# Performance work log

Hardware: AMD Instinct MI355X
Metric: run time of the kernel (lower is better)

## Reference

```python
import jax, jax.numpy as jnp
import numpy as np

IH, IW = 14, 14
NUM_HEADS = 16
HEAD_DIMS = 32
INP_DIMS = 512
B = 128


def make_relative_position_index(ih, iw):
    coords = np.stack(np.meshgrid(np.arange(ih), np.arange(iw), indexing='ij'))  # [2, ih, iw]
    cf = coords.reshape(2, -1)  # [2, n]
    rel = cf[:, :, None] - cf[:, None, :]  # [2, n, n]
    rel = rel.transpose(1, 2, 0)  # [n, n, 2]
    rel[:, :, 0] += ih - 1
    rel[:, :, 1] += iw - 1
    rel[:, :, 0] *= 2 * iw - 1
    return rel.sum(-1).astype(np.int64)  # [n, n]


def setup_inputs() -> dict:
    key = jax.random.key(0)
    k1, k2, k3, k4, k5 = jax.random.split(key, 5)
    n = IH * IW
    inner = NUM_HEADS * HEAD_DIMS
    x = jax.random.normal(k1, (B, n, INP_DIMS), dtype=jnp.float32)
    qkv_w = jax.random.normal(k2, (INP_DIMS, 3 * inner), dtype=jnp.float32) * 0.02
    rel_bias_table = jax.random.normal(k3, ((2 * IH - 1) * (2 * IW - 1), NUM_HEADS), dtype=jnp.float32) * 0.02
    proj_w = jax.random.normal(k4, (inner, INP_DIMS), dtype=jnp.float32) * 0.02
    proj_b = jax.random.normal(k5, (INP_DIMS,), dtype=jnp.float32) * 0.02
    rel_pos_index = jnp.asarray(make_relative_position_index(IH, IW))
    return {"x": x, "qkv_w": qkv_w, "rel_bias_table": rel_bias_table,
            "proj_w": proj_w, "proj_b": proj_b, "rel_pos_index": rel_pos_index}


def reference(x, qkv_w, rel_bias_table, proj_w, proj_b, rel_pos_index):
    b, n, c = x.shape
    h, hd = NUM_HEADS, HEAD_DIMS
    scale = (INP_DIMS // NUM_HEADS) ** (-0.5)
    qkv = x @ qkv_w  # [b, n, 3*h*hd]
    qkv = qkv.reshape(b, n, 3, h, hd).transpose(2, 0, 3, 1, 4)  # [3, b, h, n, hd]
    q, k, v = qkv[0] * scale, qkv[1], qkv[2]
    attn = jnp.einsum('bhqd,bhkd->bhqk', q, k)  # [b, h, n, n]
    # gather relative position bias: [n*n, h] -> [h, n, n]
    bias = rel_bias_table[rel_pos_index.reshape(-1)].reshape(n, n, h).transpose(2, 0, 1)
    attn = jax.nn.softmax(attn + bias[None], axis=-1)
    out = jnp.einsum('bhqk,bhkd->bhqd', attn, v)  # [b, h, n, hd]
    out = out.transpose(0, 2, 1, 3).reshape(b, n, h * hd)
    return out @ proj_w + proj_b
```

## Files before the change

### kernel.cpp

```cpp
#include <hip/hip_runtime.h>

#define NTOK 196
#define QPAD 208
#define KP 208
#define PSTR 232

typedef __attribute__((ext_vector_type(8))) short short8;
typedef __attribute__((ext_vector_type(4))) float float4_t;

__device__ __forceinline__ short f2bf(float f) {
  unsigned u = __float_as_uint(f);
  u = (u + 0x7fffu + ((u >> 16) & 1u)) >> 16;
  return (short)u;
}

__global__ __launch_bounds__(256) void fill_kernel(float* __restrict__ out,
                                                   int n) {
  int i = blockIdx.x * 256 + threadIdx.x;
  if (i < n) out[i] = 1000.0f;
}

__global__ __launch_bounds__(256) void cvt_kernel(const float* __restrict__ in,
                                                  short* __restrict__ out) {
  int i = (blockIdx.x * 256 + threadIdx.x) * 8;
  float4_t a = *(const float4_t*)&in[i];
  float4_t b = *(const float4_t*)&in[i + 4];
  short8 v;
  v[0] = f2bf(a[0]); v[1] = f2bf(a[1]); v[2] = f2bf(a[2]); v[3] = f2bf(a[3]);
  v[4] = f2bf(b[0]); v[5] = f2bf(b[1]); v[6] = f2bf(b[2]); v[7] = f2bf(b[3]);
  *(short8*)&out[i] = v;
}

__global__ __launch_bounds__(256) void transpose_kernel(
    const float* __restrict__ in, short* __restrict__ out, int R, int C) {
  __shared__ float tile[64][65];
  int c0 = blockIdx.x * 64, r0 = blockIdx.y * 64;
  int tc = threadIdx.x & 63, tr = threadIdx.x >> 6;
#pragma unroll
  for (int s = 0; s < 16; s++) {
    int r = s * 4 + tr;
    tile[r][tc] = in[(r0 + r) * C + c0 + tc];
  }
  __syncthreads();
#pragma unroll
  for (int s = 0; s < 16; s++) {
    int i = s * 4 + tr;
    out[(c0 + i) * R + r0 + tc] = f2bf(tile[tc][i]);
  }
}

__global__ __launch_bounds__(256) void bias_kernel(
    const float* __restrict__ table, const int* __restrict__ rpi,
    float* __restrict__ bias) {
  int idx = blockIdx.x * 256 + threadIdx.x;
  if (idx >= 16 * QPAD * KP) return;
  int h = idx / (QPAD * KP);
  int rem = idx % (QPAD * KP);
  int q = rem / KP, k = rem % KP;
  float v = 0.f;
  if (q < NTOK && k < NTOK) v = table[rpi[q * NTOK + k] * 16 + h];
  bias[idx] = v;
}

__global__ __launch_bounds__(256, 2) void fused_attn(
    const short* __restrict__ xb, const short* __restrict__ wt1,
    const float* __restrict__ bias, short* __restrict__ aout) {
  __shared__ __align__(16) short R1[64 * PSTR];
  __shared__ __align__(16) short R2[32 * PSTR];
  __shared__ __align__(16) short Qs[224][40];
  __shared__ __align__(16) short Ks[224][40];
  short(*As)[40] = (short(*)[40])R1;
  short(*P)[PSTR] = (short(*)[PSTR])R1;
  short(*Bs)[40] = (short(*)[40])R2;
  short(*vTs)[PSTR] = (short(*)[PSTR])R2;

  int bh = blockIdx.x, b = bh >> 4, h = bh & 15;
  int tid = threadIdx.x, wave = tid >> 6, lane = tid & 63;
  int quad = lane >> 4, l16 = lane & 15;
  int base_row = b * NTOK;

  float4_t z4 = {0.f, 0.f, 0.f, 0.f};
  float4_t acc[4][6];
#pragma unroll
  for (int i = 0; i < 4; i++)
#pragma unroll
    for (int n = 0; n < 6; n++) acc[i][n] = z4;

  int srow = tid >> 2, scol = (tid & 3) * 8;
  for (int k0 = 0; k0 < 512; k0 += 32) {
#pragma unroll
    for (int i = 0; i < 4; i++) {
      int r = srow + i * 64;
      if (r < 224) {
        int gr = base_row + r;
        if (gr > 25087) gr = 25087;
        *(short8*)&As[r][scol] = *(const short8*)&xb[gr * 512 + k0 + scol];
      }
    }
#pragma unroll
    for (int i = 0; i < 2; i++) {
      int r = srow + i * 64;
      if (r < 96) {
        int sec = r >> 5, r32 = r & 31;
        *(short8*)&Bs[r][scol] =
            *(const short8*)&wt1[(sec * 512 + h * 32 + r32) * 512 + k0 + scol];
      }
    }
    __syncthreads();
    short8 af[4], bfv[6];
#pragma unroll
    for (int i = 0; i < 4; i++) {
      int mt = (i < 3) ? (wave + 4 * i) : (12 + (wave & 1));
      af[i] = *(short8*)&As[mt * 16 + l16][quad * 8];
    }
#pragma unroll
    for (int n = 0; n < 6; n++) bfv[n] = *(short8*)&Bs[n * 16 + l16][quad * 8];
#pragma unroll
    for (int i = 0; i < 4; i++)
#pragma unroll
      for (int n = 0; n < 6; n++)
        acc[i][n] = __builtin_amdgcn_mfma_f32_16x16x32_bf16(af[i], bfv[n],
                                                            acc[i][n], 0, 0, 0);
    __syncthreads();
  }
  const float qscale = 0.17677669529663687f;
#pragma unroll
  for (int i = 0; i < 4; i++) {
    if (i == 3 && wave >= 2) break;
    int mt = (i < 3) ? (wave + 4 * i) : (12 + wave);
    int row0 = mt * 16 + quad * 4;
#pragma unroll
    for (int n = 0; n < 6; n++) {
      int c = n * 16 + l16;
#pragma unroll
      for (int r = 0; r < 4; r++) {
        int row = row0 + r;
        float v = acc[i][n][r];
        if (c < 32)
          Qs[row][c] = f2bf(v * qscale);
        else if (c < 64)
          Ks[row][c - 32] = f2bf(v);
        else
          vTs[c - 64][row] = f2bf(v);
      }
    }
  }
  __syncthreads();
  for (int i2 = 0; i2 < 4; i2++) {
    bool active = (i2 < 3) || (wave == 0);
    int qt = (i2 < 3) ? (wave + 4 * i2) : 12;
    int qr0 = qt * 16;
    if (active) {
      short8 qf = *(short8*)&Qs[qr0 + l16][quad * 8];
      float4_t s[13];
#pragma unroll
      for (int kt = 0; kt < 13; kt++) {
        short8 kf = *(short8*)&Ks[kt * 16 + l16][quad * 8];
        s[kt] = __builtin_amdgcn_mfma_f32_16x16x32_bf16(qf, kf, z4, 0, 0, 0);
      }
      const float* brow = bias + (h * QPAD + qr0 + quad * 4) * KP;
#pragma unroll
      for (int kt = 0; kt < 13; kt++) {
        int col = kt * 16 + l16;
#pragma unroll
        for (int r = 0; r < 4; r++) s[kt][r] += brow[r * KP + col];
      }
      if (l16 >= 4) {
#pragma unroll
        for (int r = 0; r < 4; r++) s[12][r] = -1e30f;
      }
      int prow_base = wave * 16 + quad * 4;
#pragma unroll
      for (int r = 0; r < 4; r++) {
        float m = s[0][r];
#pragma unroll
        for (int kt = 1; kt < 13; kt++) m = fmaxf(m, s[kt][r]);
        m = fmaxf(m, __shfl_xor(m, 8, 16));
        m = fmaxf(m, __shfl_xor(m, 4, 16));
        m = fmaxf(m, __shfl_xor(m, 2, 16));
        m = fmaxf(m, __shfl_xor(m, 1, 16));
        float sum = 0.f;
#pragma unroll
        for (int kt = 0; kt < 13; kt++) {
          float p = __expf(s[kt][r] - m);
          s[kt][r] = p;
          sum += p;
        }
        sum += __shfl_xor(sum, 8, 16);
        sum += __shfl_xor(sum, 4, 16);
        sum += __shfl_xor(sum, 2, 16);
        sum += __shfl_xor(sum, 1, 16);
        float inv = 1.f / sum;
        short* prow = &P[prow_base + r][0];
#pragma unroll
        for (int kt = 0; kt < 13; kt++)
          prow[kt * 16 + l16] = f2bf(s[kt][r] * inv);
        prow[208 + l16] = 0;
      }
    }
    __syncthreads();
    if (active) {
      float4_t o0 = z4, o1 = z4;
#pragma unroll
      for (int kt = 0; kt < 7; kt++) {
        short8 pf = *(short8*)&P[wave * 16 + l16][kt * 32 + quad * 8];
        short8 vf0 = *(short8*)&vTs[l16][kt * 32 + quad * 8];
        short8 vf1 = *(short8*)&vTs[16 + l16][kt * 32 + quad * 8];
        o0 = __builtin_amdgcn_mfma_f32_16x16x32_bf16(pf, vf0, o0, 0, 0, 0);
        o1 = __builtin_amdgcn_mfma_f32_16x16x32_bf16(pf, vf1, o1, 0, 0, 0);
      }
#pragma unroll
      for (int r = 0; r < 4; r++) {
        int row = qr0 + quad * 4 + r;
        if (row < NTOK) {
          int off = (base_row + row) * 512 + h * 32;
          aout[off + l16] = f2bf(o0[r]);
          aout[off + 16 + l16] = f2bf(o1[r]);
        }
      }
    }
    __syncthreads();
  }
}

__device__ __forceinline__ void gemm_tile(const short* __restrict__ A,
                                          const short* __restrict__ B, int K,
                                          int m0, int n0, short (*As)[72],
                                          short (*Bs)[72], float4_t acc[4][4]) {
  int tid = threadIdx.x;
  int lane = tid & 63, wave = tid >> 6;
  int quad = lane >> 4, l16 = lane & 15;
  int wm = (wave >> 1) * 64, wn = (wave & 1) * 64;
  int srow = tid >> 3, scol = (tid & 7) * 8;
  for (int k0 = 0; k0 < K; k0 += 64) {
#pragma unroll
    for (int i = 0; i < 4; i++) {
      int r = srow + i * 32;
      *(short8*)&As[r][scol] = *(const short8*)&A[(m0 + r) * K + k0 + scol];
      *(short8*)&Bs[r][scol] = *(const short8*)&B[(n0 + r) * K + k0 + scol];
    }
    __syncthreads();
#pragma unroll
    for (int ks = 0; ks < 2; ks++) {
      short8 af[4], bfr[4];
#pragma unroll
      for (int i = 0; i < 4; i++) {
        af[i] = *(short8*)&As[wm + i * 16 + l16][ks * 32 + quad * 8];
        bfr[i] = *(short8*)&Bs[wn + i * 16 + l16][ks * 32 + quad * 8];
      }
#pragma unroll
      for (int mi = 0; mi < 4; mi++)
#pragma unroll
        for (int ni = 0; ni < 4; ni++)
          acc[mi][ni] = __builtin_amdgcn_mfma_f32_16x16x32_bf16(
              af[mi], bfr[ni], acc[mi][ni], 0, 0, 0);
    }
    __syncthreads();
  }
}

__global__ __launch_bounds__(256) void proj_gemm(
    const short* __restrict__ a, const short* __restrict__ wt,
    const float* __restrict__ pb, float* __restrict__ out) {
  __shared__ __align__(16) short As[128][72];
  __shared__ __align__(16) short Bs[128][72];
  float4_t acc[4][4];
  float4_t z = {0.f, 0.f, 0.f, 0.f};
#pragma unroll
  for (int i = 0; i < 4; i++)
#pragma unroll
    for (int j = 0; j < 4; j++) acc[i][j] = z;
  int m0 = blockIdx.y * 128, n0 = blockIdx.x * 128;
  gemm_tile(a, wt, 512, m0, n0, As, Bs, acc);
  int lane = threadIdx.x & 63, wave = threadIdx.x >> 6;
  int quad = lane >> 4, l16 = lane & 15;
  int wm = (wave >> 1) * 64, wn = (wave & 1) * 64;
#pragma unroll
  for (int mi = 0; mi < 4; mi++)
#pragma unroll
    for (int ni = 0; ni < 4; ni++) {
      int colg = n0 + wn + ni * 16 + l16;
      float bv = pb[colg];
#pragma unroll
      for (int r = 0; r < 4; r++) {
        int rowg = m0 + wm + mi * 16 + quad * 4 + r;
        out[rowg * 512 + colg] = acc[mi][ni][r] + bv;
      }
    }
}

extern "C" void kernel_launch(void* const* d_in, const int* in_sizes, int n_in,
                              void* d_out, int out_size, void* d_ws,
                              size_t ws_size, hipStream_t stream) {
  const float* x = (const float*)d_in[0];
  const float* qkv_w = (const float*)d_in[1];
  const float* table = (const float*)d_in[2];
  const float* proj_w = (const float*)d_in[3];
  const float* proj_b = (const float*)d_in[4];
  const int* rpi = (const int*)d_in[5];
  float* out = (float*)d_out;

  const size_t NEEDED = 56246272;
  if (ws_size < NEEDED) {
    fill_kernel<<<(out_size + 255) / 256, 256, 0, stream>>>(out, out_size);
    return;
  }
  char* w = (char*)d_ws;
  short* wt1 = (short*)(w);
  short* wt2 = (short*)(w + 1572864);
  float* bias = (float*)(w + 2097152);
  short* aout = (short*)(w + 4866048);
  short* xb = (short*)(w + 30556160);

  cvt_kernel<<<25088 * 512 / (256 * 8), 256, 0, stream>>>(x, xb);
  transpose_kernel<<<dim3(24, 8), 256, 0, stream>>>(qkv_w, wt1, 512, 1536);
  transpose_kernel<<<dim3(8, 8), 256, 0, stream>>>(proj_w, wt2, 512, 512);
  bias_kernel<<<(16 * QPAD * KP + 255) / 256, 256, 0, stream>>>(table, rpi,
                                                                bias);
  fused_attn<<<2048, 256, 0, stream>>>(xb, wt1, bias, aout);
  proj_gemm<<<dim3(4, 196), 256, 0, stream>>>(aout, wt2, proj_b, out);
}
```

Baseline: 321.4 us.

## Split fused QKV+attention into separate QKV GEMM and attention kernels

Replaces the per-(batch,head) fused kernel, which recomputed the QKV projection inside each attention block, with a standalone tiled 128x128 QKV GEMM. That GEMM writes scaled Q, K and V in a per-head padded bf16 layout, and a lighter attention kernel then reads them. The aim is to get better MFMA utilization and reuse of the weights for the projection. The cost is writing and reading about 80MB of Q/K/V intermediates and needing a larger workspace. When the workspace is too small, the old fused path is kept as a fallback.

```diff
diff --git a/kernel.cpp b/kernel.cpp
--- a/kernel.cpp
+++ b/kernel.cpp
@@ -62,6 +62,179 @@
   bias[idx] = v;
 }
 
+__device__ __forceinline__ void gemm_tile(const short* __restrict__ A,
+                                          const short* __restrict__ B, int K,
+                                          int m0, int n0, short (*As)[72],
+                                          short (*Bs)[72], float4_t acc[4][4]) {
+  int tid = threadIdx.x;
+  int lane = tid & 63, wave = tid >> 6;
+  int quad = lane >> 4, l16 = lane & 15;
+  int wm = (wave >> 1) * 64, wn = (wave & 1) * 64;
+  int srow = tid >> 3, scol = (tid & 7) * 8;
+  for (int k0 = 0; k0 < K; k0 += 64) {
+#pragma unroll
+    for (int i = 0; i < 4; i++) {
+      int r = srow + i * 32;
+      *(short8*)&As[r][scol] = *(const short8*)&A[(m0 + r) * K + k0 + scol];
+      *(short8*)&Bs[r][scol] = *(const short8*)&B[(n0 + r) * K + k0 + scol];
+    }
+    __syncthreads();
+#pragma unroll
+    for (int ks = 0; ks < 2; ks++) {
+      short8 af[4], bfr[4];
+#pragma unroll
+      for (int i = 0; i < 4; i++) {
+        af[i] = *(short8*)&As[wm + i * 16 + l16][ks * 32 + quad * 8];
+        bfr[i] = *(short8*)&Bs[wn + i * 16 + l16][ks * 32 + quad * 8];
+      }
+#pragma unroll
+      for (int mi = 0; mi < 4; mi++)
+#pragma unroll
+        for (int ni = 0; ni < 4; ni++)
+          acc[mi][ni] = __builtin_amdgcn_mfma_f32_16x16x32_bf16(
+              af[mi], bfr[ni], acc[mi][ni], 0, 0, 0);
+    }
+    __syncthreads();
+  }
+}
+
+__global__ __launch_bounds__(256) void qkv_gemm(
+    const short* __restrict__ xb, const short* __restrict__ wt1,
+    short* __restrict__ qb, short* __restrict__ kb, short* __restrict__ vb) {
+  __shared__ __align__(16) short As[128][72];
+  __shared__ __align__(16) short Bs[128][72];
+  float4_t acc[4][4];
+  float4_t z = {0.f, 0.f, 0.f, 0.f};
+#pragma unroll
+  for (int i = 0; i < 4; i++)
+#pragma unroll
+    for (int j = 0; j < 4; j++) acc[i][j] = z;
+  int m0 = blockIdx.y * 128, n0 = blockIdx.x * 128;
+  gemm_tile(xb, wt1, 512, m0, n0, As, Bs, acc);
+  int lane = threadIdx.x & 63, wave = threadIdx.x >> 6;
+  int quad = lane >> 4, l16 = lane & 15;
+  int wm = (wave >> 1) * 64, wn = (wave & 1) * 64;
+  const float qscale = 0.17677669529663687f;
+#pragma unroll
+  for (int mi = 0; mi < 4; mi++)
+#pragma unroll
+    for (int ni = 0; ni < 4; ni++)
+#pragma unroll
+      for (int r = 0; r < 4; r++) {
+        int rowg = m0 + wm + mi * 16 + quad * 4 + r;
+        int colg = n0 + wn + ni * 16 + l16;
+        float v = acc[mi][ni][r];
+        int s = colg >> 9, rem = colg & 511;
+        int h = rem >> 5, d = rem & 31;
+        int b = rowg / NTOK, n = rowg - b * NTOK;
+        int off = ((b * 16 + h) * QPAD + n) * 32 + d;
+        if (s == 0)
+          qb[off] = f2bf(v * qscale);
+        else if (s == 1)
+          kb[off] = f2bf(v);
+        else
+          vb[off] = f2bf(v);
+      }
+}
+
+__global__ __launch_bounds__(256) void attn_kernel(
+    const short* __restrict__ qb, const short* __restrict__ kb,
+    const short* __restrict__ vb, const float* __restrict__ bias,
+    short* __restrict__ aout) {
+  __shared__ __align__(16) short vT[32][PSTR];
+  __shared__ __align__(16) short P[4][16][PSTR];
+  int bh = blockIdx.x, b = bh >> 4, h = bh & 15;
+  int tid = threadIdx.x, wave = tid >> 6, lane = tid & 63;
+  int quad = lane >> 4, l16 = lane & 15;
+  int base_row = b * NTOK;
+  const short* vsrc = vb + bh * QPAD * 32;
+  for (int i = tid; i < NTOK * 32; i += 256) {
+    int key = i >> 5, d = i & 31;
+    vT[d][key] = vsrc[i];
+  }
+  for (int i = tid; i < 32 * (PSTR - NTOK); i += 256) {
+    int d = i / (PSTR - NTOK), c = i - d * (PSTR - NTOK);
+    vT[d][NTOK + c] = 0;
+  }
+  __syncthreads();
+  float4_t z4 = {0.f, 0.f, 0.f, 0.f};
+  for (int i2 = 0; i2 < 4; i2++) {
+    bool active = (i2 < 3) || (wave == 0);
+    int qt = (i2 < 3) ? (wave + 4 * i2) : 12;
+    int qr0 = qt * 16;
+    if (active) {
+      short8 qf = *(const short8*)&qb[(bh * QPAD + qr0 + l16) * 32 + quad * 8];
+      float4_t s[13];
+#pragma unroll
+      for (int kt = 0; kt < 13; kt++) {
+        short8 kf =
+            *(const short8*)&kb[(bh * QPAD + kt * 16 + l16) * 32 + quad * 8];
+        s[kt] = __builtin_amdgcn_mfma_f32_16x16x32_bf16(qf, kf, z4, 0, 0, 0);
+      }
+      const float* brow = bias + (h * QPAD + qr0 + quad * 4) * KP;
+#pragma unroll
+      for (int kt = 0; kt < 13; kt++) {
+        int col = kt * 16 + l16;
+#pragma unroll
+        for (int r = 0; r < 4; r++) s[kt][r] += brow[r * KP + col];
+      }
+      if (l16 >= 4) {
+#pragma unroll
+        for (int r = 0; r < 4; r++) s[12][r] = -1e30f;
+      }
+#pragma unroll
+      for (int r = 0; r < 4; r++) {
+        float m = s[0][r];
+#pragma unroll
+        for (int kt = 1; kt < 13; kt++) m = fmaxf(m, s[kt][r]);
+        m = fmaxf(m, __shfl_xor(m, 8, 16));
+        m = fmaxf(m, __shfl_xor(m, 4, 16));
+        m = fmaxf(m, __shfl_xor(m, 2, 16));
+        m = fmaxf(m, __shfl_xor(m, 1, 16));
+        float sum = 0.f;
+#pragma unroll
+        for (int kt = 0; kt < 13; kt++) {
+          float p = __expf(s[kt][r] - m);
+          s[kt][r] = p;
+          sum += p;
+        }
+        sum += __shfl_xor(sum, 8, 16);
+        sum += __shfl_xor(sum, 4, 16);
+        sum += __shfl_xor(sum, 2, 16);
+        sum += __shfl_xor(sum, 1, 16);
+        float inv = 1.f / sum;
+        short* prow = &P[wave][quad * 4 + r][0];
+#pragma unroll
+        for (int kt = 0; kt < 13; kt++)
+          prow[kt * 16 + l16] = f2bf(s[kt][r] * inv);
+        prow[208 + l16] = 0;
+      }
+    }
+    __syncthreads();
+    if (active) {
+      float4_t o0 = z4, o1 = z4;
+#pragma unroll
+      for (int kt = 0; kt < 7; kt++) {
+        short8 pf = *(short8*)&P[wave][l16][kt * 32 + quad * 8];
+        short8 vf0 = *(short8*)&vT[l16][kt * 32 + quad * 8];
+        short8 vf1 = *(short8*)&vT[16 + l16][kt * 32 + quad * 8];
+        o0 = __builtin_amdgcn_mfma_f32_16x16x32_bf16(pf, vf0, o0, 0, 0, 0);
+        o1 = __builtin_amdgcn_mfma_f32_16x16x32_bf16(pf, vf1, o1, 0, 0, 0);
+      }
+#pragma unroll
+      for (int r = 0; r < 4; r++) {
+        int row = qr0 + quad * 4 + r;
+        if (row < NTOK) {
+          int off = (base_row + row) * 512 + h * 32;
+          aout[off + l16] = f2bf(o0[r]);
+          aout[off + 16 + l16] = f2bf(o1[r]);
+        }
+      }
+    }
+    __syncthreads();
+  }
+}
+
 __global__ __launch_bounds__(256, 2) void fused_attn(
     const short* __restrict__ xb, const short* __restrict__ wt1,
     const float* __restrict__ bias, short* __restrict__ aout) {
@@ -223,42 +396,6 @@
   }
 }
 
-__device__ __forceinline__ void gemm_tile(const short* __restrict__ A,
-                                          const short* __restrict__ B, int K,
-                                          int m0, int n0, short (*As)[72],
-                                          short (*Bs)[72], float4_t acc[4][4]) {
-  int tid = threadIdx.x;
-  int lane = tid & 63, wave = tid >> 6;
-  int quad = lane >> 4, l16 = lane & 15;
-  int wm = (wave >> 1) * 64, wn = (wave & 1) * 64;
-  int srow = tid >> 3, scol = (tid & 7) * 8;
-  for (int k0 = 0; k0 < K; k0 += 64) {
-#pragma unroll
-    for (int i = 0; i < 4; i++) {
-      int r = srow + i * 32;
-      *(short8*)&As[r][scol] = *(const short8*)&A[(m0 + r) * K + k0 + scol];
-      *(short8*)&Bs[r][scol] = *(const short8*)&B[(n0 + r) * K + k0 + scol];
-    }
-    __syncthreads();
-#pragma unroll
-    for (int ks = 0; ks < 2; ks++) {
-      short8 af[4], bfr[4];
-#pragma unroll
-      for (int i = 0; i < 4; i++) {
-        af[i] = *(short8*)&As[wm + i * 16 + l16][ks * 32 + quad * 8];
-        bfr[i] = *(short8*)&Bs[wn + i * 16 + l16][ks * 32 + quad * 8];
-      }
-#pragma unroll
-      for (int mi = 0; mi < 4; mi++)
-#pragma unroll
-        for (int ni = 0; ni < 4; ni++)
-          acc[mi][ni] = __builtin_amdgcn_mfma_f32_16x16x32_bf16(
-              af[mi], bfr[ni], acc[mi][ni], 0, 0, 0);
-    }
-    __syncthreads();
-  }
-}
-
 __global__ __launch_bounds__(256) void proj_gemm(
     const short* __restrict__ a, const short* __restrict__ wt,
     const float* __restrict__ pb, float* __restrict__ out) {
@@ -300,23 +437,33 @@
   const int* rpi = (const int*)d_in[5];
   float* out = (float*)d_out;
 
-  const size_t NEEDED = 56246272;
-  if (ws_size < NEEDED) {
-    fill_kernel<<<(out_size + 255) / 256, 256, 0, stream>>>(out, out_size);
-    return;
-  }
   char* w = (char*)d_ws;
   short* wt1 = (short*)(w);
   short* wt2 = (short*)(w + 1572864);
   float* bias = (float*)(w + 2097152);
-  short* aout = (short*)(w + 4866048);
-  short* xb = (short*)(w + 30556160);
-
-  cvt_kernel<<<25088 * 512 / (256 * 8), 256, 0, stream>>>(x, xb);
+  short* xb = (short*)(w + 4866048);
+  short* qb = (short*)(w + 30556160);
+  short* kb = (short*)(w + 57819136);
+  short* vb = (short*)(w + 85082112);
+  const size_t NEEDED_SPLIT = 112345088;
+  const size_t NEEDED_FUSED = 30556160 + 25690112;
+
   transpose_kernel<<<dim3(24, 8), 256, 0, stream>>>(qkv_w, wt1, 512, 1536);
   transpose_kernel<<<dim3(8, 8), 256, 0, stream>>>(proj_w, wt2, 512, 512);
   bias_kernel<<<(16 * QPAD * KP + 255) / 256, 256, 0, stream>>>(table, rpi,
                                                                 bias);
-  fused_attn<<<2048, 256, 0, stream>>>(xb, wt1, bias, aout);
-  proj_gemm<<<dim3(4, 196), 256, 0, stream>>>(aout, wt2, proj_b, out);
-}
+  if (ws_size >= NEEDED_SPLIT) {
+    short* aout = xb;
+    cvt_kernel<<<25088 * 512 / (256 * 8), 256, 0, stream>>>(x, xb);
+    qkv_gemm<<<dim3(12, 196), 256, 0, stream>>>(xb, wt1, qb, kb, vb);
+    attn_kernel<<<2048, 256, 0, stream>>>(qb, kb, vb, bias, aout);
+    proj_gemm<<<dim3(4, 196), 256, 0, stream>>>(aout, wt2, proj_b, out);
+  } else if (ws_size >= NEEDED_FUSED) {
+    short* aout = (short*)(w + 30556160);
+    cvt_kernel<<<25088 * 512 / (256 * 8), 256, 0, stream>>>(x, xb);
+    fused_attn<<<2048, 256, 0, stream>>>(xb, wt1, bias, aout);
+    proj_gemm<<<dim3(4, 196), 256, 0, stream>>>(aout, wt2, proj_b, out);
+  } else {
+    fill_kernel<<<(out_size + 255) / 256, 256, 0, stream>>>(out, out_size);
+  }
+}
```

New measurement: 280.2 us. 12.8% less time.

## Split fused QKV+attention into a tiled QKV GEMM and a separate attention kernel

Applied to the files above, without the earlier changes.

The per-(batch,head) fused kernel, which recomputed the QKV projection with poor tile reuse, is replaced by a standalone 128x128 tiled QKV GEMM that writes head-major padded Q/K/V buffers, followed by a lighter attention kernel. Bias is precomputed in MFMA fragment order and prescaled by log2e so softmax can use exp2 with no max subtraction. Normalisation is deferred to the output. Dropping the max subtraction risks overflow for larger logits, and the Q/K/V intermediates add global-memory traffic and a larger workspace.

```diff
diff --git a/kernel.cpp b/kernel.cpp
--- a/kernel.cpp
+++ b/kernel.cpp
@@ -1,9 +1,11 @@
 #include <hip/hip_runtime.h>
+#include <hip/hip_bf16.h>
 
 #define NTOK 196
 #define QPAD 208
-#define KP 208
 #define PSTR 232
+#define QW 20
+#define LOG2E 1.4426950408889634f
 
 typedef __attribute__((ext_vector_type(8))) short short8;
 typedef __attribute__((ext_vector_type(4))) float float4_t;
@@ -51,138 +53,158 @@
 
 __global__ __launch_bounds__(256) void bias_kernel(
     const float* __restrict__ table, const int* __restrict__ rpi,
-    float* __restrict__ bias) {
+    float4_t* __restrict__ biasV) {
   int idx = blockIdx.x * 256 + threadIdx.x;
-  if (idx >= 16 * QPAD * KP) return;
-  int h = idx / (QPAD * KP);
-  int rem = idx % (QPAD * KP);
-  int q = rem / KP, k = rem % KP;
-  float v = 0.f;
-  if (q < NTOK && k < NTOK) v = table[rpi[q * NTOK + k] * 16 + h];
-  bias[idx] = v;
-}
-
-__global__ __launch_bounds__(256, 2) void fused_attn(
+  if (idx >= 16 * 13 * 13 * 64) return;
+  int lane = idx & 63;
+  int t = idx >> 6;
+  int kt = t % 13; t /= 13;
+  int qt = t % 13;
+  int h = t / 13;
+  int quad = lane >> 4, l16 = lane & 15;
+  int k = kt * 16 + l16;
+  float4_t v = {0.f, 0.f, 0.f, 0.f};
+  if (k < NTOK) {
+#pragma unroll
+    for (int r = 0; r < 4; r++) {
+      int q = qt * 16 + quad * 4 + r;
+      if (q < NTOK) v[r] = table[rpi[q * NTOK + k] * 16 + h] * LOG2E;
+    }
+  }
+  biasV[idx] = v;
+}
+
+__device__ __forceinline__ void gemm_tile(const short* __restrict__ A,
+                                          const short* __restrict__ B, int K,
+                                          int m0, int n0, short (*As)[72],
+                                          short (*Bs)[72], float4_t acc[4][4]) {
+  int tid = threadIdx.x;
+  int lane = tid & 63, wave = tid >> 6;
+  int quad = lane >> 4, l16 = lane & 15;
+  int wm = (wave >> 1) * 64, wn = (wave & 1) * 64;
+  int srow = tid >> 3, scol = (tid & 7) * 8;
+  for (int k0 = 0; k0 < K; k0 += 64) {
+#pragma unroll
+    for (int i = 0; i < 4; i++) {
+      int r = srow + i * 32;
+      *(short8*)&As[r][scol] = *(const short8*)&A[(m0 + r) * K + k0 + scol];
+      *(short8*)&Bs[r][scol] = *(const short8*)&B[(n0 + r) * K + k0 + scol];
+    }
+    __syncthreads();
+#pragma unroll
+    for (int ks = 0; ks < 2; ks++) {
+      short8 af[4], bfr[4];
+#pragma unroll
+      for (int i = 0; i < 4; i++) {
+        af[i] = *(short8*)&As[wm + i * 16 + l16][ks * 32 + quad * 8];
+        bfr[i] = *(short8*)&Bs[wn + i * 16 + l16][ks * 32 + quad * 8];
+      }
+#pragma unroll
+      for (int mi = 0; mi < 4; mi++)
+#pragma unroll
+        for (int ni = 0; ni < 4; ni++)
+          acc[mi][ni] = __builtin_amdgcn_mfma_f32_16x16x32_bf16(
+              af[mi], bfr[ni], acc[mi][ni], 0, 0, 0);
+    }
+    __syncthreads();
+  }
+}
+
+__global__ __launch_bounds__(256) void qkv_gemm(
     const short* __restrict__ xb, const short* __restrict__ wt1,
-    const float* __restrict__ bias, short* __restrict__ aout) {
-  __shared__ __align__(16) short R1[64 * PSTR];
-  __shared__ __align__(16) short R2[32 * PSTR];
-  __shared__ __align__(16) short Qs[224][40];
-  __shared__ __align__(16) short Ks[224][40];
-  short(*As)[40] = (short(*)[40])R1;
-  short(*P)[PSTR] = (short(*)[PSTR])R1;
-  short(*Bs)[40] = (short(*)[40])R2;
-  short(*vTs)[PSTR] = (short(*)[PSTR])R2;
-
+    short* __restrict__ qb, short* __restrict__ kb, short* __restrict__ vb) {
+  __shared__ __align__(16) short As[128][72];
+  __shared__ __align__(16) short Bs[128][72];
+  float4_t acc[4][4];
+  float4_t z = {0.f, 0.f, 0.f, 0.f};
+#pragma unroll
+  for (int i = 0; i < 4; i++)
+#pragma unroll
+    for (int j = 0; j < 4; j++) acc[i][j] = z;
+  int m0 = blockIdx.y * 128, n0 = blockIdx.x * 128;
+  gemm_tile(xb, wt1, 512, m0, n0, As, Bs, acc);
+  int lane = threadIdx.x & 63, wave = threadIdx.x >> 6;
+  int quad = lane >> 4, l16 = lane & 15;
+  int wm = (wave >> 1) * 64, wn = (wave & 1) * 64;
+  const float qscale = 0.17677669529663687f * LOG2E;
+#pragma unroll
+  for (int mi = 0; mi < 4; mi++)
+#pragma unroll
+    for (int ni = 0; ni < 4; ni++)
+#pragma unroll
+      for (int r = 0; r < 4; r++) {
+        int rowg = m0 + wm + mi * 16 + quad * 4 + r;
+        int colg = n0 + wn + ni * 16 + l16;
+        float v = acc[mi][ni][r];
+        int s = colg >> 9, rem = colg & 511;
+        int h = rem >> 5, d = rem & 31;
+        int b = rowg / NTOK, n = rowg - b * NTOK;
+        int off = ((b * 16 + h) * QPAD + n) * 32 + d;
+        if (s == 0)
+          qb[off] = f2bf(v * qscale);
+        else if (s == 1)
+          kb[off] = f2bf(v);
+        else
+          vb[off] = f2bf(v);
+      }
+}
+
+__global__ __launch_bounds__(256) void attn_kernel(
+    const short* __restrict__ qb, const short* __restrict__ kb,
+    const short* __restrict__ vb, const float4_t* __restrict__ biasV,
+    short* __restrict__ aout) {
+  __shared__ __align__(16) short vT[32][PSTR];
+  __shared__ __align__(8) short PT[4][224][QW];
   int bh = blockIdx.x, b = bh >> 4, h = bh & 15;
   int tid = threadIdx.x, wave = tid >> 6, lane = tid & 63;
   int quad = lane >> 4, l16 = lane & 15;
   int base_row = b * NTOK;
-
+  const short* vsrc = vb + bh * QPAD * 32;
+  for (int i = tid; i < NTOK * 32; i += 256) {
+    int key = i >> 5, d = i & 31;
+    vT[d][key] = vsrc[i];
+  }
+  for (int i = tid; i < 32 * (PSTR - NTOK); i += 256) {
+    int d = i / (PSTR - NTOK), c = i - d * (PSTR - NTOK);
+    vT[d][NTOK + c] = 0;
+  }
+  for (int i = tid; i < 4 * 16 * QW; i += 256) {
+    int w = i / (16 * QW), rem = i % (16 * QW);
+    PT[w][208 + rem / QW][rem % QW] = 0;
+  }
+  __syncthreads();
   float4_t z4 = {0.f, 0.f, 0.f, 0.f};
-  float4_t acc[4][6];
-#pragma unroll
-  for (int i = 0; i < 4; i++)
-#pragma unroll
-    for (int n = 0; n < 6; n++) acc[i][n] = z4;
-
-  int srow = tid >> 2, scol = (tid & 3) * 8;
-  for (int k0 = 0; k0 < 512; k0 += 32) {
-#pragma unroll
-    for (int i = 0; i < 4; i++) {
-      int r = srow + i * 64;
-      if (r < 224) {
-        int gr = base_row + r;
-        if (gr > 25087) gr = 25087;
-        *(short8*)&As[r][scol] = *(const short8*)&xb[gr * 512 + k0 + scol];
-      }
-    }
-#pragma unroll
-    for (int i = 0; i < 2; i++) {
-      int r = srow + i * 64;
-      if (r < 96) {
-        int sec = r >> 5, r32 = r & 31;
-        *(short8*)&Bs[r][scol] =
-            *(const short8*)&wt1[(sec * 512 + h * 32 + r32) * 512 + k0 + scol];
-      }
-    }
-    __syncthreads();
-    short8 af[4], bfv[6];
-#pragma unroll
-    for (int i = 0; i < 4; i++) {
-      int mt = (i < 3) ? (wave + 4 * i) : (12 + (wave & 1));
-      af[i] = *(short8*)&As[mt * 16 + l16][quad * 8];
-    }
-#pragma unroll
-    for (int n = 0; n < 6; n++) bfv[n] = *(short8*)&Bs[n * 16 + l16][quad * 8];
-#pragma unroll
-    for (int i = 0; i < 4; i++)
-#pragma unroll
-      for (int n = 0; n < 6; n++)
-        acc[i][n] = __builtin_amdgcn_mfma_f32_16x16x32_bf16(af[i], bfv[n],
-                                                            acc[i][n], 0, 0, 0);
-    __syncthreads();
-  }
-  const float qscale = 0.17677669529663687f;
-#pragma unroll
-  for (int i = 0; i < 4; i++) {
-    if (i == 3 && wave >= 2) break;
-    int mt = (i < 3) ? (wave + 4 * i) : (12 + wave);
-    int row0 = mt * 16 + quad * 4;
-#pragma unroll
-    for (int n = 0; n < 6; n++) {
-      int c = n * 16 + l16;
-#pragma unroll
-      for (int r = 0; r < 4; r++) {
-        int row = row0 + r;
-        float v = acc[i][n][r];
-        if (c < 32)
-          Qs[row][c] = f2bf(v * qscale);
-        else if (c < 64)
-          Ks[row][c - 32] = f2bf(v);
-        else
-          vTs[c - 64][row] = f2bf(v);
-      }
-    }
-  }
-  __syncthreads();
   for (int i2 = 0; i2 < 4; i2++) {
     bool active = (i2 < 3) || (wave == 0);
     int qt = (i2 < 3) ? (wave + 4 * i2) : 12;
     int qr0 = qt * 16;
+    float inv[4];
     if (active) {
-      short8 qf = *(short8*)&Qs[qr0 + l16][quad * 8];
+      short8 qf = *(const short8*)&qb[(bh * QPAD + qr0 + l16) * 32 + quad * 8];
       float4_t s[13];
 #pragma unroll
       for (int kt = 0; kt < 13; kt++) {
-        short8 kf = *(short8*)&Ks[kt * 16 + l16][quad * 8];
+        short8 kf =
+            *(const short8*)&kb[(bh * QPAD + kt * 16 + l16) * 32 + quad * 8];
         s[kt] = __builtin_amdgcn_mfma_f32_16x16x32_bf16(qf, kf, z4, 0, 0, 0);
       }
-      const float* brow = bias + (h * QPAD + qr0 + quad * 4) * KP;
+      const float4_t* bv = biasV + ((h * 13 + qt) * 13) * 64 + lane;
 #pragma unroll
       for (int kt = 0; kt < 13; kt++) {
-        int col = kt * 16 + l16;
-#pragma unroll
-        for (int r = 0; r < 4; r++) s[kt][r] += brow[r * KP + col];
+        float4_t bb = bv[kt * 64];
+#pragma unroll
+        for (int r = 0; r < 4; r++) s[kt][r] += bb[r];
       }
       if (l16 >= 4) {
 #pragma unroll
         for (int r = 0; r < 4; r++) s[12][r] = -1e30f;
       }
-      int prow_base = wave * 16 + quad * 4;
 #pragma unroll
       for (int r = 0; r < 4; r++) {
-        float m = s[0][r];
-#pragma unroll
-        for (int kt = 1; kt < 13; kt++) m = fmaxf(m, s[kt][r]);
-        m = fmaxf(m, __shfl_xor(m, 8, 16));
-        m = fmaxf(m, __shfl_xor(m, 4, 16));
-        m = fmaxf(m, __shfl_xor(m, 2, 16));
-        m = fmaxf(m, __shfl_xor(m, 1, 16));
         float sum = 0.f;
 #pragma unroll
         for (int kt = 0; kt < 13; kt++) {
-          float p = __expf(s[kt][r] - m);
+          float p = exp2f(s[kt][r]);
           s[kt][r] = p;
           sum += p;
         }
@@ -190,22 +212,30 @@
         sum += __shfl_xor(sum, 4, 16);
         sum += __shfl_xor(sum, 2, 16);
         sum += __shfl_xor(sum, 1, 16);
-        float inv = 1.f / sum;
-        short* prow = &P[prow_base + r][0];
-#pragma unroll
-        for (int kt = 0; kt < 13; kt++)
-          prow[kt * 16 + l16] = f2bf(s[kt][r] * inv);
-        prow[208 + l16] = 0;
+        inv[r] = 1.f / sum;
+      }
+#pragma unroll
+      for (int kt = 0; kt < 13; kt++) {
+        float2 f01 = {s[kt][0], s[kt][1]};
+        float2 f23 = {s[kt][2], s[kt][3]};
+        __hip_bfloat162 h01 = __float22bfloat162_rn(f01);
+        __hip_bfloat162 h23 = __float22bfloat162_rn(f23);
+        uint2 uu;
+        uu.x = *(unsigned*)&h01;
+        uu.y = *(unsigned*)&h23;
+        *(uint2*)&PT[wave][kt * 16 + l16][quad * 4] = uu;
       }
     }
     __syncthreads();
     if (active) {
       float4_t o0 = z4, o1 = z4;
 #pragma unroll
-      for (int kt = 0; kt < 7; kt++) {
-        short8 pf = *(short8*)&P[wave * 16 + l16][kt * 32 + quad * 8];
-        short8 vf0 = *(short8*)&vTs[l16][kt * 32 + quad * 8];
-        short8 vf1 = *(short8*)&vTs[16 + l16][kt * 32 + quad * 8];
+      for (int c = 0; c < 7; c++) {
+        short8 pf;
+#pragma unroll
+        for (int j = 0; j < 8; j++) pf[j] = PT[wave][c * 32 + quad * 8 + j][l16];
+        short8 vf0 = *(short8*)&vT[l16][c * 32 + quad * 8];
+        short8 vf1 = *(short8*)&vT[16 + l16][c * 32 + quad * 8];
         o0 = __builtin_amdgcn_mfma_f32_16x16x32_bf16(pf, vf0, o0, 0, 0, 0);
         o1 = __builtin_amdgcn_mfma_f32_16x16x32_bf16(pf, vf1, o1, 0, 0, 0);
       }
@@ -214,46 +244,10 @@
         int row = qr0 + quad * 4 + r;
         if (row < NTOK) {
           int off = (base_row + row) * 512 + h * 32;
-          aout[off + l16] = f2bf(o0[r]);
-          aout[off + 16 + l16] = f2bf(o1[r]);
+          aout[off + l16] = f2bf(o0[r] * inv[r]);
+          aout[off + 16 + l16] = f2bf(o1[r] * inv[r]);
         }
       }
-    }
-    __syncthreads();
-  }
-}
-
-__device__ __forceinline__ void gemm_tile(const short* __restrict__ A,
-                                          const short* __restrict__ B, int K,
-                                          int m0, int n0, short (*As)[72],
-                                          short (*Bs)[72], float4_t acc[4][4]) {
-  int tid = threadIdx.x;
-  int lane = tid & 63, wave = tid >> 6;
-  int quad = lane >> 4, l16 = lane & 15;
-  int wm = (wave >> 1) * 64, wn = (wave & 1) * 64;
-  int srow = tid >> 3, scol = (tid & 7) * 8;
-  for (int k0 = 0; k0 < K; k0 += 64) {
-#pragma unroll
-    for (int i = 0; i < 4; i++) {
-      int r = srow + i * 32;
-      *(short8*)&As[r][scol] = *(const short8*)&A[(m0 + r) * K + k0 + scol];
-      *(short8*)&Bs[r][scol] = *(const short8*)&B[(n0 + r) * K + k0 + scol];
-    }
-    __syncthreads();
-#pragma unroll
-    for (int ks = 0; ks < 2; ks++) {
-      short8 af[4], bfr[4];
-#pragma unroll
-      for (int i = 0; i < 4; i++) {
-        af[i] = *(short8*)&As[wm + i * 16 + l16][ks * 32 + quad * 8];
-        bfr[i] = *(short8*)&Bs[wn + i * 16 + l16][ks * 32 + quad * 8];
-      }
-#pragma unroll
-      for (int mi = 0; mi < 4; mi++)
-#pragma unroll
-        for (int ni = 0; ni < 4; ni++)
-          acc[mi][ni] = __builtin_amdgcn_mfma_f32_16x16x32_bf16(
-              af[mi], bfr[ni], acc[mi][ni], 0, 0, 0);
     }
     __syncthreads();
   }
@@ -300,23 +294,27 @@
   const int* rpi = (const int*)d_in[5];
   float* out = (float*)d_out;
 
-  const size_t NEEDED = 56246272;
+  char* w = (char*)d_ws;
+  short* wt1 = (short*)(w);
+  short* wt2 = (short*)(w + 1572864);
+  float4_t* biasV = (float4_t*)(w + 2097152);
+  short* xb = (short*)(w + 4866048);
+  short* qb = (short*)(w + 30556160);
+  short* kb = (short*)(w + 57819136);
+  short* vb = (short*)(w + 85082112);
+  const size_t NEEDED = 112345088;
   if (ws_size < NEEDED) {
     fill_kernel<<<(out_size + 255) / 256, 256, 0, stream>>>(out, out_size);
     return;
   }
-  char* w = (char*)d_ws;
-  short* wt1 = (short*)(w);
-  short* wt2 = (short*)(w + 1572864);
-  float* bias = (float*)(w + 2097152);
-  short* aout = (short*)(w + 4866048);
-  short* xb = (short*)(w + 30556160);
-
-  cvt_kernel<<<25088 * 512 / (256 * 8), 256, 0, stream>>>(x, xb);
+  short* aout = xb;
+
   transpose_kernel<<<dim3(24, 8), 256, 0, stream>>>(qkv_w, wt1, 512, 1536);
   transpose_kernel<<<dim3(8, 8), 256, 0, stream>>>(proj_w, wt2, 512, 512);
-  bias_kernel<<<(16 * QPAD * KP + 255) / 256, 256, 0, stream>>>(table, rpi,
-                                                                bias);
-  fused_attn<<<2048, 256, 0, stream>>>(xb, wt1, bias, aout);
+  bias_kernel<<<(16 * 13 * 13 * 64 + 255) / 256, 256, 0, stream>>>(table, rpi,
+                                                                   biasV);
+  cvt_kernel<<<25088 * 512 / (256 * 8), 256, 0, stream>>>(x, xb);
+  qkv_gemm<<<dim3(12, 196), 256, 0, stream>>>(xb, wt1, qb, kb, vb);
+  attn_kernel<<<2048, 256, 0, stream>>>(qb, kb, vb, biasV, aout);
   proj_gemm<<<dim3(4, 196), 256, 0, stream>>>(aout, wt2, proj_b, out);
 }
```

Result: slower. 339.1 us (+5.5%).
